# Kernel tuning notes

Hardware: AMD Instinct MI355X
Metric: run time of the kernel (lower is better)

Reference implementation:

```python
import jax, jax.numpy as jnp
import numpy as np

B, T, K, D = 32, 512, 4, 256
E, M = 100000, 2048
NEG = -10000000000.0


def setup_inputs() -> dict:
    key = jax.random.key(0)
    ks = jax.random.split(key, 8)
    token_reprs = jax.random.normal(ks[0], (B, T, K, D), dtype=jnp.float32)
    edge_index = jax.random.randint(ks[1], (2, E), 0, B * T, dtype=jnp.int64)
    lm_indices = jax.random.randint(ks[2], (M,), 0, B * T * K, dtype=jnp.int64)
    batch_pointers = jax.random.randint(ks[3], (M,), 0, B, dtype=jnp.int64)
    tree_padding_mask = jax.random.bernoulli(ks[4], 0.8, (B, T))
    # SwiGLU(2*dim, 4*dim, 1) parameters (no biases)
    sg = 1.0 / np.sqrt(2 * D)
    sh = 1.0 / np.sqrt(4 * D)
    Wg = jax.random.normal(ks[5], (2 * D, 4 * D), dtype=jnp.float32) * sg
    Wv = jax.random.normal(ks[6], (2 * D, 4 * D), dtype=jnp.float32) * sg
    Wo = jax.random.normal(ks[7], (4 * D, 1), dtype=jnp.float32) * sh
    return {
        "token_reprs": token_reprs,
        "Wg": Wg,
        "Wv": Wv,
        "Wo": Wo,
        "edge_index": edge_index,
        "lm_indices": lm_indices,
        "batch_pointers": batch_pointers,
        "tree_padding_mask": tree_padding_mask,
    }


def reference(token_reprs, Wg, Wv, Wo, edge_index, lm_indices, batch_pointers, tree_padding_mask):
    b, t, k, d = token_reprs.shape
    # predict_lemmas: gather type reprs via edge_index, concat, SwiGLU MLP
    type_flat = token_reprs[:, :, 0].reshape(b * t, d)           # [B*T, D]
    scope_ids, goal_ids = edge_index[0], edge_index[1]
    x = jnp.concatenate([type_flat[scope_ids], type_flat[goal_ids]], axis=-1)  # [E, 2D]
    h = jax.nn.silu(x @ Wg) * (x @ Wv)                           # [E, 4D]
    lemmas = (h @ Wo).squeeze(-1)                                # [E]
    # predict_masks: gathers + masked dot-product scoring
    mask_reprs = token_reprs.reshape(-1, d)[lm_indices]          # [M, D]
    type_reprs = token_reprs[:, :, 0]                            # [B, T, D]
    candidates = type_reprs[batch_pointers]                      # [M, T, D]
    candidate_mask = tree_padding_mask[batch_pointers]           # [M, T]
    lm_preds = jnp.einsum('md,mtd->mt', mask_reprs, candidates)  # [M, T]
    lm_preds = jnp.where(candidate_mask, lm_preds, NEG)
    return lemmas, lm_preds
```

## Files before the change

### kernel.cpp

```cpp
#include <hip/hip_runtime.h>
#include <hip/hip_bf16.h>

typedef __bf16 bf16x8 __attribute__((ext_vector_type(8)));
typedef int   i32x8 __attribute__((ext_vector_type(8)));
typedef float f32x4 __attribute__((ext_vector_type(4)));

#define KDIM 512
#define NDIM 1024
#define DDIM 256
#define TDIM 512
#define MDIM 2048
#define NROWS 16384
#define NEGV -1e10f
#define NLM 128
#define WARR 524288

__device__ __forceinline__ unsigned int pk8(float a, float b, float c, float d) {
    unsigned int p = (unsigned int)__builtin_amdgcn_cvt_pk_fp8_f32(a, b, 0, 0);
    return (unsigned int)__builtin_amdgcn_cvt_pk_fp8_f32(c, d, (int)p, 1);
}

typedef const __attribute__((address_space(1))) unsigned int* gas_p;
typedef __attribute__((address_space(3))) unsigned int* las_p;
__device__ __forceinline__ void gl2lds16(const void* g, void* l) {
    __builtin_amdgcn_global_load_lds((gas_p)g, (las_p)l, 16, 0, 0);
}

__global__ void prep_all(const float* __restrict__ tok,
                         const float* __restrict__ Wg,
                         const float* __restrict__ Wv,
                         const int* __restrict__ bp,
                         unsigned char* __restrict__ tf8,
                         unsigned char* __restrict__ wp8,
                         int* __restrict__ counts,
                         unsigned short* __restrict__ lists) {
    const int bid = blockIdx.x;
    const int tid = threadIdx.x;
    if (bid < 4096) {
        int g = (bid * 256 + tid) * 4;
        int i = g >> 8, c = g & 255;
        float4 v = *(const float4*)(tok + (size_t)i * 1024 + c);
        *(unsigned int*)(tf8 + g) = pk8(v.x, v.y, v.z, v.w);
    } else if (bid < 4608) {
        __shared__ float tg[32][33];
        __shared__ float tv[32][33];
        int pb = bid - 4096;
        int n0 = (pb & 31) * 32, k0 = (pb >> 5) * 32;
        {
            int kk = tid >> 3, nn = (tid & 7) * 4;
            float4 g = *(const float4*)(Wg + (size_t)(k0 + kk) * NDIM + n0 + nn);
            float4 v = *(const float4*)(Wv + (size_t)(k0 + kk) * NDIM + n0 + nn);
            tg[kk][nn] = g.x; tg[kk][nn + 1] = g.y; tg[kk][nn + 2] = g.z; tg[kk][nn + 3] = g.w;
            tv[kk][nn] = v.x; tv[kk][nn + 1] = v.y; tv[kk][nn + 2] = v.z; tv[kk][nn + 3] = v.w;
        }
        __syncthreads();
        int nn2 = tid >> 3, kk2 = (tid & 7) * 4;
        unsigned int pg = pk8(tg[kk2][nn2], tg[kk2 + 1][nn2],
                              tg[kk2 + 2][nn2], tg[kk2 + 3][nn2]);
        unsigned int pv = pk8(tv[kk2][nn2], tv[kk2 + 1][nn2],
                              tv[kk2 + 2][nn2], tv[kk2 + 3][nn2]);
        int n = n0 + nn2, k = k0 + kk2;
        int nt = n >> 6, wn = (n >> 5) & 1, ni = (n >> 4) & 1, cp = n & 15;
        int kc = k >> 7, rem = k & 127, qq = rem >> 5, hh = (rem >> 4) & 1, bb = rem & 15;
        int frag = ((nt * 4 + kc) * 2 + wn) * 2 + ni;
        size_t off = (size_t)frag * 2048 + (qq * 16 + cp) * 32 + hh * 16 + bb;
        *(unsigned int*)(wp8 + off) = pg;
        *(unsigned int*)(wp8 + WARR + off) = pv;
    } else {
        __shared__ int c[32];
        if (tid < 32) c[tid] = 0;
        __syncthreads();
        for (int m = tid; m < MDIM; m += 256) {
            int b = bp[m];
            int pos = atomicAdd(&c[b], 1);
            lists[b * MDIM + pos] = (unsigned short)m;
        }
        __syncthreads();
        if (tid < 32) counts[tid] = c[tid];
    }
}

__launch_bounds__(256, 2)
__global__ void fused_main(const unsigned char* __restrict__ tf8,
                           const unsigned char* __restrict__ wp8,
                           const float* __restrict__ Wo,
                           const int* __restrict__ scope,
                           const int* __restrict__ goal,
                           float* __restrict__ outLem, int E,
                           const float* __restrict__ tok,
                           const int* __restrict__ lmi,
                           const int* __restrict__ counts,
                           const unsigned short* __restrict__ lists,
                           const int* __restrict__ tpm,
                           float* __restrict__ outP) {
    __shared__ unsigned char sA[64 * 1024];
    __shared__ float sRed[256];

    const int tid = threadIdx.x;
    const int lane = tid & 63;
    const int w = tid >> 6;
    const int col = lane & 15;
    const int q = lane >> 4;

    if ((int)blockIdx.x < NLM) {
        const int lb = blockIdx.x;
        const int b = lb & 31;
        const int t0 = (lb >> 5) * 128;
        const int cnt = counts[b];
        for (int mt = w * 16; mt < cnt; mt += 64) {
            int mc = mt + col;
            int aid = lists[b * MDIM + (mc < cnt ? mc : cnt - 1)];
            const float* arow = tok + (size_t)lmi[aid] * DDIM;
            i32x8 af[2];
#pragma unroll
            for (int kc = 0; kc < 2; kc++) {
                unsigned int d[8];
#pragma unroll
                for (int j = 0; j < 8; j++) {
                    float4 v = *(const float4*)(arow + kc * 128 + q * 32 + j * 4);
                    d[j] = pk8(v.x, v.y, v.z, v.w);
                }
                af[kc] = (i32x8){(int)d[0], (int)d[1], (int)d[2], (int)d[3],
                                 (int)d[4], (int)d[5], (int)d[6], (int)d[7]};
            }
            int gm[4];
#pragma unroll
            for (int r = 0; r < 4; r++) {
                int mrow = mt + q * 4 + r;
                gm[r] = (mrow < cnt) ? (int)lists[b * MDIM + mrow] : -1;
            }
#pragma unroll
            for (int ntile = 0; ntile < 8; ntile++) {
                int t = t0 + ntile * 16 + col;
                const unsigned char* brow = tf8 + (size_t)(b * TDIM + t) * DDIM;
                f32x4 acc = (f32x4){0.f, 0.f, 0.f, 0.f};
#pragma unroll
                for (int kc = 0; kc < 2; kc++) {
                    uint4 lo = *(const uint4*)(brow + kc * 128 + q * 32);
                    uint4 hi = *(const uint4*)(brow + kc * 128 + q * 32 + 16);
                    i32x8 bf = (i32x8){(int)lo.x, (int)lo.y, (int)lo.z, (int)lo.w,
                                       (int)hi.x, (int)hi.y, (int)hi.z, (int)hi.w};
                    acc = __builtin_amdgcn_mfma_scale_f32_16x16x128_f8f6f4(
                        af[kc], bf, acc, 0, 0, 0, 0x7F7F7F7F, 0, 0x7F7F7F7F);
                }
                int pmv = tpm[b * TDIM + t];
#pragma unroll
                for (int r = 0; r < 4; r++) {
                    if (gm[r] >= 0)
                        outP[(size_t)gm[r] * TDIM + t] = pmv ? acc[r] : NEGV;
                }
            }
        }
        return;
    }

    const int bx = blockIdx.x - NLM;
    const int etile = bx * 128;
    const int wm = w & 1;
    const int wn = w >> 1;

#pragma unroll
    for (int i = 0; i < 16; i++) {
        int r = w * 16 + i;
        int j = r & 1, kc = (r >> 1) & 3, mi = (r >> 3) & 3, am = r >> 5;
        int row = am * 64 + mi * 16 + col;
        int e = etile + row;
        int id = (e < E) ? ((kc < 2) ? scope[e] : goal[e]) : 0;
        gl2lds16(tf8 + (size_t)id * DDIM + (kc & 1) * 128 + q * 32 + j * 16,
                 &sA[r * 1024]);
    }
    __syncthreads();

    float lem[16];
#pragma unroll
    for (int i = 0; i < 16; i++) lem[i] = 0.f;

    const unsigned char* wbase = wp8 + lane * 32;

#define LOADB(s, buf)                                                          \
    {                                                                          \
        _Pragma("unroll")                                                      \
        for (int ni_ = 0; ni_ < 2; ni_++) {                                    \
            size_t f_ = (size_t)(((s) * 2 + wn) * 2 + ni_) * 2048;             \
            uint4 lo_ = *(const uint4*)(wbase + f_);                           \
            uint4 hi_ = *(const uint4*)(wbase + f_ + 16);                      \
            bgb[buf][ni_] = (i32x8){(int)lo_.x, (int)lo_.y, (int)lo_.z,        \
                (int)lo_.w, (int)hi_.x, (int)hi_.y, (int)hi_.z, (int)hi_.w};   \
            lo_ = *(const uint4*)(wbase + WARR + f_);                          \
            hi_ = *(const uint4*)(wbase + WARR + f_ + 16);                     \
            bvb[buf][ni_] = (i32x8){(int)lo_.x, (int)lo_.y, (int)lo_.z,        \
                (int)lo_.w, (int)hi_.x, (int)hi_.y, (int)hi_.z, (int)hi_.w};   \
        }                                                                      \
    }

    i32x8 bgb[2][2], bvb[2][2];
    LOADB(0, 0)

    for (int nt = 0; nt < 16; nt++) {
        f32x4 accG[4][2], accV[4][2];
#pragma unroll
        for (int mi = 0; mi < 4; mi++)
#pragma unroll
            for (int ni = 0; ni < 2; ni++) {
                accG[mi][ni] = (f32x4){0.f, 0.f, 0.f, 0.f};
                accV[mi][ni] = (f32x4){0.f, 0.f, 0.f, 0.f};
            }
#pragma unroll
        for (int kc = 0; kc < 4; kc++) {
            const int cur = kc & 1, nxt = cur ^ 1;
            LOADB(nt * 4 + kc + 1, nxt)
#pragma unroll
            for (int mi = 0; mi < 4; mi++) {
                int rb = ((wm * 4 + mi) * 4 + kc) * 2;
                uint4 lo = *(const uint4*)(&sA[rb * 1024 + lane * 16]);
                uint4 hi = *(const uint4*)(&sA[(rb + 1) * 1024 + lane * 16]);
                i32x8 af = (i32x8){(int)lo.x, (int)lo.y, (int)lo.z, (int)lo.w,
                                   (int)hi.x, (int)hi.y, (int)hi.z, (int)hi.w};
#pragma unroll
                for (int ni = 0; ni < 2; ni++) {
                    accG[mi][ni] = __builtin_amdgcn_mfma_scale_f32_16x16x128_f8f6f4(
                        af, bgb[cur][ni], accG[mi][ni], 0, 0, 0,
                        0x7F7F7F7F, 0, 0x7F7F7F7F);
                    accV[mi][ni] = __builtin_amdgcn_mfma_scale_f32_16x16x128_f8f6f4(
                        af, bvb[cur][ni], accV[mi][ni], 0, 0, 0,
                        0x7F7F7F7F, 0, 0x7F7F7F7F);
                }
            }
        }
#pragma unroll
        for (int ni = 0; ni < 2; ni++) {
            float wo = Wo[nt * 64 + wn * 32 + ni * 16 + col];
#pragma unroll
            for (int mi = 0; mi < 4; mi++)
#pragma unroll
                for (int r = 0; r < 4; r++) {
                    float g = accG[mi][ni][r];
                    float v = accV[mi][ni][r];
                    float s = g * __builtin_amdgcn_rcpf(1.f + __expf(-g));
                    lem[mi * 4 + r] += s * v * wo;
                }
        }
    }
#pragma unroll
    for (int i = 0; i < 16; i++) {
        float v = lem[i];
        for (int off = 8; off > 0; off >>= 1) v += __shfl_xor(v, off, 16);
        if (col == 0) {
            int row = wm * 64 + (i >> 2) * 16 + q * 4 + (i & 3);
            sRed[wn * 128 + row] = v;
        }
    }
    __syncthreads();
    if (tid < 128) {
        int e = etile + tid;
        if (e < E) outLem[e] = sRed[tid] + sRed[128 + tid];
    }
}

extern "C" void kernel_launch(void* const* d_in, const int* in_sizes, int n_in,
                              void* d_out, int out_size, void* d_ws, size_t ws_size,
                              hipStream_t stream) {
    const float* tok = (const float*)d_in[0];
    const float* Wg  = (const float*)d_in[1];
    const float* Wv  = (const float*)d_in[2];
    const float* Wo  = (const float*)d_in[3];
    const int* edge = (const int*)d_in[4];
    const int* lmi  = (const int*)d_in[5];
    const int* bp   = (const int*)d_in[6];
    const int* tpm  = (const int*)d_in[7];
    const int E = in_sizes[4] / 2;
    float* out = (float*)d_out;

    unsigned char* tf8 = (unsigned char*)d_ws;
    unsigned char* wp8 = tf8 + (size_t)NROWS * DDIM;
    int* counts = (int*)(wp8 + 2 * WARR);
    unsigned short* lists = (unsigned short*)(counts + 32);

    prep_all<<<dim3(4609), dim3(256), 0, stream>>>(
        tok, Wg, Wv, bp, tf8, wp8, counts, lists);
    int nLemBlocks = (E + 127) / 128;
    fused_main<<<dim3(NLM + nLemBlocks), dim3(256), 0, stream>>>(
        tf8, wp8, Wo, edge, edge + E, out, E,
        tok, lmi, counts, lists, tpm, out + E);
}
```

Baseline: 229.8 us.

## Give each wave 32 edge rows and the full N range, dropping cross-wave reduction

Changes the warp tiling of the SwiGLU GEMM so that each of the four waves owns 32 distinct edge rows and iterates over all 64 output columns of each N tile, instead of a 2x2 split over 64 rows and 32 columns. Each wave now reads only its own A fragments from LDS, and the per-row lemma sum completes inside the wave. That removes the shared-memory reduction buffer, the final __syncthreads and the two-way combine. The trade-off is that every wave now streams all of the Wg/Wv fp8 weight fragments from global memory, doubling per-wave B traffic and register prefetch volume, while LDS A reads per MFMA are reduced.

```diff
diff --git a/kernel.cpp b/kernel.cpp
--- a/kernel.cpp
+++ b/kernel.cpp
@@ -94,7 +94,6 @@
                            const int* __restrict__ tpm,
                            float* __restrict__ outP) {
     __shared__ unsigned char sA[64 * 1024];
-    __shared__ float sRed[256];
 
     const int tid = threadIdx.x;
     const int lane = tid & 63;
@@ -156,14 +155,12 @@
 
     const int bx = blockIdx.x - NLM;
     const int etile = bx * 128;
-    const int wm = w & 1;
-    const int wn = w >> 1;
 
 #pragma unroll
     for (int i = 0; i < 16; i++) {
         int r = w * 16 + i;
-        int j = r & 1, kc = (r >> 1) & 3, mi = (r >> 3) & 3, am = r >> 5;
-        int row = am * 64 + mi * 16 + col;
+        int j = i & 1, kc = (i >> 1) & 3, mi = (i >> 3) & 1;
+        int row = w * 32 + mi * 16 + col;
         int e = etile + row;
         int id = (e < E) ? ((kc < 2) ? scope[e] : goal[e]) : 0;
         gl2lds16(tf8 + (size_t)id * DDIM + (kc & 1) * 128 + q * 32 + j * 16,
@@ -171,17 +168,17 @@
     }
     __syncthreads();
 
-    float lem[16];
-#pragma unroll
-    for (int i = 0; i < 16; i++) lem[i] = 0.f;
+    float lem[8];
+#pragma unroll
+    for (int i = 0; i < 8; i++) lem[i] = 0.f;
 
     const unsigned char* wbase = wp8 + lane * 32;
 
-#define LOADB(s, buf)                                                          \
+#define LOADB(t, buf)                                                          \
     {                                                                          \
         _Pragma("unroll")                                                      \
         for (int ni_ = 0; ni_ < 2; ni_++) {                                    \
-            size_t f_ = (size_t)(((s) * 2 + wn) * 2 + ni_) * 2048;             \
+            size_t f_ = (size_t)((t) * 2 + ni_) * 2048;                        \
             uint4 lo_ = *(const uint4*)(wbase + f_);                           \
             uint4 hi_ = *(const uint4*)(wbase + f_ + 16);                      \
             bgb[buf][ni_] = (i32x8){(int)lo_.x, (int)lo_.y, (int)lo_.z,        \
@@ -197,63 +194,69 @@
     LOADB(0, 0)
 
     for (int nt = 0; nt < 16; nt++) {
-        f32x4 accG[4][2], accV[4][2];
-#pragma unroll
-        for (int mi = 0; mi < 4; mi++)
-#pragma unroll
-            for (int ni = 0; ni < 2; ni++) {
-                accG[mi][ni] = (f32x4){0.f, 0.f, 0.f, 0.f};
-                accV[mi][ni] = (f32x4){0.f, 0.f, 0.f, 0.f};
-            }
+        f32x4 accG[2][2][2], accV[2][2][2];
+#pragma unroll
+        for (int mi = 0; mi < 2; mi++)
+#pragma unroll
+            for (int nh = 0; nh < 2; nh++)
+#pragma unroll
+                for (int ni = 0; ni < 2; ni++) {
+                    accG[mi][nh][ni] = (f32x4){0.f, 0.f, 0.f, 0.f};
+                    accV[mi][nh][ni] = (f32x4){0.f, 0.f, 0.f, 0.f};
+                }
 #pragma unroll
         for (int kc = 0; kc < 4; kc++) {
-            const int cur = kc & 1, nxt = cur ^ 1;
-            LOADB(nt * 4 + kc + 1, nxt)
-#pragma unroll
-            for (int mi = 0; mi < 4; mi++) {
-                int rb = ((wm * 4 + mi) * 4 + kc) * 2;
+            i32x8 af[2];
+#pragma unroll
+            for (int mi = 0; mi < 2; mi++) {
+                int rb = ((w * 2 + mi) * 4 + kc) * 2;
                 uint4 lo = *(const uint4*)(&sA[rb * 1024 + lane * 16]);
                 uint4 hi = *(const uint4*)(&sA[(rb + 1) * 1024 + lane * 16]);
-                i32x8 af = (i32x8){(int)lo.x, (int)lo.y, (int)lo.z, (int)lo.w,
-                                   (int)hi.x, (int)hi.y, (int)hi.z, (int)hi.w};
-#pragma unroll
-                for (int ni = 0; ni < 2; ni++) {
-                    accG[mi][ni] = __builtin_amdgcn_mfma_scale_f32_16x16x128_f8f6f4(
-                        af, bgb[cur][ni], accG[mi][ni], 0, 0, 0,
-                        0x7F7F7F7F, 0, 0x7F7F7F7F);
-                    accV[mi][ni] = __builtin_amdgcn_mfma_scale_f32_16x16x128_f8f6f4(
-                        af, bvb[cur][ni], accV[mi][ni], 0, 0, 0,
-                        0x7F7F7F7F, 0, 0x7F7F7F7F);
-                }
-            }
-        }
-#pragma unroll
-        for (int ni = 0; ni < 2; ni++) {
-            float wo = Wo[nt * 64 + wn * 32 + ni * 16 + col];
-#pragma unroll
-            for (int mi = 0; mi < 4; mi++)
-#pragma unroll
-                for (int r = 0; r < 4; r++) {
-                    float g = accG[mi][ni][r];
-                    float v = accV[mi][ni][r];
-                    float s = g * __builtin_amdgcn_rcpf(1.f + __expf(-g));
-                    lem[mi * 4 + r] += s * v * wo;
-                }
-        }
-    }
-#pragma unroll
-    for (int i = 0; i < 16; i++) {
+                af[mi] = (i32x8){(int)lo.x, (int)lo.y, (int)lo.z, (int)lo.w,
+                                 (int)hi.x, (int)hi.y, (int)hi.z, (int)hi.w};
+            }
+#pragma unroll
+            for (int nh = 0; nh < 2; nh++) {
+                const int t = (nt * 4 + kc) * 2 + nh;
+                const int cur = t & 1, nxt = cur ^ 1;
+                LOADB(t + 1, nxt)
+#pragma unroll
+                for (int mi = 0; mi < 2; mi++)
+#pragma unroll
+                    for (int ni = 0; ni < 2; ni++) {
+                        accG[mi][nh][ni] = __builtin_amdgcn_mfma_scale_f32_16x16x128_f8f6f4(
+                            af[mi], bgb[cur][ni], accG[mi][nh][ni], 0, 0, 0,
+                            0x7F7F7F7F, 0, 0x7F7F7F7F);
+                        accV[mi][nh][ni] = __builtin_amdgcn_mfma_scale_f32_16x16x128_f8f6f4(
+                            af[mi], bvb[cur][ni], accV[mi][nh][ni], 0, 0, 0,
+                            0x7F7F7F7F, 0, 0x7F7F7F7F);
+                    }
+            }
+        }
+#pragma unroll
+        for (int nh = 0; nh < 2; nh++)
+#pragma unroll
+            for (int ni = 0; ni < 2; ni++) {
+                float wo = Wo[nt * 64 + nh * 32 + ni * 16 + col];
+#pragma unroll
+                for (int mi = 0; mi < 2; mi++)
+#pragma unroll
+                    for (int r = 0; r < 4; r++) {
+                        float g = accG[mi][nh][ni][r];
+                        float v = accV[mi][nh][ni][r];
+                        float s = g * __builtin_amdgcn_rcpf(1.f + __expf(-g));
+                        lem[mi * 4 + r] += s * v * wo;
+                    }
+            }
+    }
+#pragma unroll
+    for (int i = 0; i < 8; i++) {
         float v = lem[i];
         for (int off = 8; off > 0; off >>= 1) v += __shfl_xor(v, off, 16);
         if (col == 0) {
-            int row = wm * 64 + (i >> 2) * 16 + q * 4 + (i & 3);
-            sRed[wn * 128 + row] = v;
-        }
-    }
-    __syncthreads();
-    if (tid < 128) {
-        int e = etile + tid;
-        if (e < E) outLem[e] = sRed[tid] + sRed[128 + tid];
+            int e = etile + w * 32 + (i >> 2) * 16 + q * 4 + (i & 3);
+            if (e < E) outLem[e] = v;
+        }
     }
 }
 
```

New measurement: 244.6 us. 1.06x slower.
